# Performance work log

Hardware: AMD Instinct MI355X
Metric: run time of the kernel (lower is better)

The kernel has to match this reference:

```python
import jax, jax.numpy as jnp
import numpy as np

N, C, T = 8, 256, 512
H, KQ, OUT = 8, 256, 256
EPS = 1e-5


def sym_linear(x, w, stride):
    # w: (2, out_dim); circulant-grouped expansion to (2T, out_dim), then x @ cp
    out_dim = w.shape[1]
    idx = (jnp.arange(out_dim)[None, :] - jnp.arange(T)[:, None] * stride) % out_dim  # (T, out_dim)
    cp = w[:, idx].transpose(1, 0, 2).reshape(2 * T, out_dim)  # cat of rolled copies
    return x @ cp


def ln2d(x, g, b):
    # LayerNorm over last two dims (T, 2T) with affine params (T, 2T)
    mu = jnp.mean(x, axis=(-2, -1), keepdims=True)
    var = jnp.mean(jnp.square(x - mu), axis=(-2, -1), keepdims=True)
    return (x - mu) / jnp.sqrt(var + EPS) * g + b


def setup_inputs() -> dict:
    key = jax.random.key(0)
    ks = jax.random.split(key, 16)
    stdv = 1.0 / np.sqrt(2 * T)
    u = lambda k, shape, s: jax.random.uniform(k, shape, jnp.float32, -s, s)
    return {
        "x": jax.random.normal(ks[0], (N, C, T), jnp.float32),
        "Wq": u(ks[1], (KQ, C), 1.0 / np.sqrt(C)),
        "Wk": u(ks[2], (KQ, C), 1.0 / np.sqrt(C)),
        "Wv": u(ks[3], (OUT, C), 1.0 / np.sqrt(C)),
        "m1w0": u(ks[4], (2, 2 * T), stdv),
        "m2w0": u(ks[5], (2, 2 * T), stdv),
        "m1w1": u(ks[6], (2, 2 * T), stdv),
        "m2w1": u(ks[7], (2, T), stdv),
        "ln1g0": 1.0 + 0.1 * jax.random.normal(ks[8], (T, 2 * T), jnp.float32),
        "ln1b0": 0.1 * jax.random.normal(ks[9], (T, 2 * T), jnp.float32),
        "ln2g0": 1.0 + 0.1 * jax.random.normal(ks[10], (T, 2 * T), jnp.float32),
        "ln2b0": 0.1 * jax.random.normal(ks[11], (T, 2 * T), jnp.float32),
        "ln1g1": 1.0 + 0.1 * jax.random.normal(ks[12], (T, 2 * T), jnp.float32),
        "ln1b1": 0.1 * jax.random.normal(ks[13], (T, 2 * T), jnp.float32),
    }


def reference(x, Wq, Wk, Wv, m1w0, m2w0, m1w1, m2w1,
              ln1g0, ln1b0, ln2g0, ln2b0, ln1g1, ln1b1):
    dk = KQ // H
    q = jnp.einsum('oc,nct->not', Wq, x).reshape(N, H, dk, T).transpose(0, 1, 3, 2)  # (N,H,T,dk)
    k = jnp.einsum('oc,nct->not', Wk, x).reshape(N, H, dk, T)                        # (N,H,dk,T)
    v = jnp.einsum('oc,nct->not', Wv, x).reshape(N, H, OUT // H, T).transpose(0, 1, 3, 2)  # (N,H,T,dv)

    scores = jnp.einsum('nhtd,nhds->nhts', q, k) / np.sqrt(dk)  # (N,H,T,T)
    ar = jnp.arange(T, dtype=jnp.float32)
    pd = jnp.abs(ar[None, :] - ar[:, None]) / (T - 1)  # (T,T)
    p = jnp.stack([scores, jnp.broadcast_to(pd, scores.shape)], axis=-1)  # (N,H,T,T,2)
    p = p.reshape(N, H, T, 2 * T)

    def transpose_pairs(z):
        return z.reshape(N, H, T, T, 2).transpose(0, 1, 3, 2, 4)

    # mix block 0 (intermediate)
    p = ln2d(sym_linear(p, m1w0, 2), ln1g0, ln1b0)
    p = jax.nn.gelu(transpose_pairs(p), approximate=False).reshape(N, H, T, 2 * T)
    p = ln2d(sym_linear(p, m2w0, 2), ln2g0, ln2b0)
    p = jax.nn.gelu(transpose_pairs(p), approximate=False).reshape(N, H, T, 2 * T)

    # mix block 1 (final)
    p = ln2d(sym_linear(p, m1w1, 2), ln1g1, ln1b1)
    p = jax.nn.gelu(transpose_pairs(p), approximate=False).reshape(N, H, T, 2 * T)
    p = sym_linear(p, m2w1, 1)           # (N,H,T,T), out_roll_stride = T // T * 1
    p = p.transpose(0, 1, 3, 2)

    attn = jax.nn.softmax(p, axis=-1)
    out = jnp.einsum('nhts,nhsd->nhtd', attn, v)  # (N,H,T,dv)
    return out.transpose(0, 1, 3, 2).reshape(N, OUT, T)
```

## Files before the change

### kernel.cpp

```cpp
#include <hip/hip_runtime.h>
#include <hip/hip_bf16.h>
#include <math.h>

#define CDIM 256
#define TDIM 512
#define T2   1024
#define NB   64
#define MTOT 524288.0f

typedef __bf16 bf16x8 __attribute__((ext_vector_type(8)));
typedef float  f32x4  __attribute__((ext_vector_type(4)));
typedef ushort ushort8v __attribute__((ext_vector_type(8)));
typedef ushort ushort4v __attribute__((ext_vector_type(4)));

__device__ __forceinline__ ushort f2bf(float f) {
  union { float f; unsigned u; } v; v.f = f;
  unsigned r = v.u + 0x7fffu + ((v.u >> 16) & 1u);
  return (ushort)(r >> 16);
}
__device__ __forceinline__ float bf2f(ushort h) {
  union { unsigned u; float f; } v; v.u = ((unsigned)h) << 16;
  return v.f;
}
__device__ __forceinline__ float gelu_exact(float x) {
  return 0.5f * x * (1.0f + erff(x * 0.7071067811865475f));
}

#define TO_LDS(p)  ((__attribute__((address_space(3))) void*)(unsigned)(uintptr_t)(p))
#define TO_GLB(p)  ((const __attribute__((address_space(1))) void*)(uintptr_t)(p))
#define GLOAD_LDS16(g, l) __builtin_amdgcn_global_load_lds(TO_GLB(g), TO_LDS(l), 16, 0, 0)

#define BAR()    asm volatile("s_barrier" ::: "memory")
#define WAITL()  asm volatile("s_waitcnt lgkmcnt(0)" ::: "memory")
#define WAITV4() asm volatile("s_waitcnt vmcnt(4)" ::: "memory")
#define WAITV0() asm volatile("s_waitcnt vmcnt(0)" ::: "memory")

__global__ __launch_bounds__(256)
void proj_kernel(const float* __restrict__ x, const float* __restrict__ Wq,
                 const float* __restrict__ Wk, const float* __restrict__ Wv,
                 ushort* __restrict__ qb, ushort* __restrict__ kb,
                 float* __restrict__ vp) {
  int t = blockIdx.x * 256 + threadIdx.x;
  int o = blockIdx.y;
  int n = blockIdx.z;
  const float* xn = x + (long)n * CDIM * TDIM;
  float aq = 0.f, ak = 0.f, av = 0.f;
  for (int c = 0; c < CDIM; ++c) {
    float xv = xn[c * TDIM + t];
    aq = fmaf(Wq[o * CDIM + c], xv, aq);
    ak = fmaf(Wk[o * CDIM + c], xv, ak);
    av = fmaf(Wv[o * CDIM + c], xv, av);
  }
  int h = o >> 5, d = o & 31;
  long bidx = (((long)(n * 8 + h) * 512) + t) * 32 + d;
  qb[bidx] = f2bf(aq);
  kb[bidx] = f2bf(ak);
  vp[((long)n * 256 + o) * TDIM + t] = av;
}

__global__ __launch_bounds__(256)
void prep_kernel(const float* __restrict__ m1w0, const float* __restrict__ m2w0,
                 const float* __restrict__ m1w1, const float* __restrict__ m2w1,
                 ushort* __restrict__ cpte0, ushort* __restrict__ cpto0,
                 ushort* __restrict__ cpt1, ushort* __restrict__ cpt2,
                 ushort* __restrict__ cpt3, ushort* __restrict__ pdb) {
  long i = (long)blockIdx.x * 256 + threadIdx.x;
  if (i < 524288) {
    int o = (int)(i >> 9), s = (int)(i & 511);
    int idx = (o - 2 * s) & 1023;
    cpte0[i] = f2bf(m1w0[idx]);
    cpto0[i] = f2bf(m1w0[1024 + idx]);
  } else if (i < 1572864) {
    long j = i - 524288;
    int o = (int)(j >> 10), kk = (int)(j & 1023);
    cpt1[j] = f2bf(m2w0[(kk & 1) * 1024 + ((o - 2 * (kk >> 1)) & 1023)]);
  } else if (i < 2621440) {
    long j = i - 1572864;
    int o = (int)(j >> 10), kk = (int)(j & 1023);
    cpt2[j] = f2bf(m1w1[(kk & 1) * 1024 + ((o - 2 * (kk >> 1)) & 1023)]);
  } else if (i < 3145728) {
    long j = i - 2621440;
    int o = (int)(j >> 10), kk = (int)(j & 1023);
    cpt3[j] = f2bf(m2w1[(kk & 1) * 512 + ((o - (kk >> 1)) & 511)]);
  } else if (i < 3407872) {
    long j = i - 3145728;
    int t = (int)(j >> 9), s = (int)(j & 511);
    pdb[j] = f2bf(fabsf((float)(s - t)) * (1.0f / 511.0f));
  }
}

__global__ __launch_bounds__(256)
void prep2_kernel(const float* __restrict__ g0, const float* __restrict__ b0,
                  const float* __restrict__ g1, const float* __restrict__ b1,
                  const float* __restrict__ g2, const float* __restrict__ b2,
                  ushort* __restrict__ gbb0, ushort* __restrict__ gbb1,
                  ushort* __restrict__ gbb2) {
  long i = (long)blockIdx.x * 256 + threadIdx.x;
  int set = (int)(i >> 18);
  long j = i & 262143;
  const float* g = set == 0 ? g0 : (set == 1 ? g1 : g2);
  const float* b = set == 0 ? b0 : (set == 1 ? b1 : b2);
  ushort* gbb    = set == 0 ? gbb0 : (set == 1 ? gbb1 : gbb2);
  float2 gv = *(const float2*)(g + 2 * j);
  float2 bv = *(const float2*)(b + 2 * j);
  ushort4v o; o[0] = f2bf(gv.x); o[1] = f2bf(bv.x); o[2] = f2bf(gv.y); o[3] = f2bf(bv.y);
  *(ushort4v*)(gbb + 4 * j) = o;
}

__global__ __launch_bounds__(256)
void scores_kernel(const ushort* __restrict__ qb, const ushort* __restrict__ kb,
                   ushort* __restrict__ S) {
  int tb = blockIdx.x;
  int b  = blockIdx.y;
  int wv = threadIdx.x >> 6, lane = threadIdx.x & 63;
  int fr = lane & 15, fq = lane >> 4;
  int t0 = tb * 64 + wv * 16;
  bf16x8 af = *(const bf16x8*)(qb + ((long)b * 512 + t0 + fr) * 32 + fq * 8);
  const ushort* kbase = kb + (long)b * 512 * 32 + fr * 32 + fq * 8;
  ushort* Sb = S + ((long)b * 512 + t0 + fq * 4) * 512 + fr;
  f32x4 zz = {0.f, 0.f, 0.f, 0.f};
#pragma unroll 4
  for (int st = 0; st < 32; ++st) {
    bf16x8 bfv = *(const bf16x8*)(kbase + st * 512);
    f32x4 acc = __builtin_amdgcn_mfma_f32_16x16x32_bf16(af, bfv, zz, 0, 0, 0);
#pragma unroll
    for (int r = 0; r < 4; ++r)
      Sb[(long)r * 512 + st * 16] = f2bf(acc[r] * 0.17677669529663687f);
  }
}

#define LDS_BUF  65536
#define LDS_BOFF 32768

#define STAGE_A_(buf, h, kt) do { \
  const ushort* gA0_ = Ab + (long)((h)*128 +      sr0) * K + (kt)*64 + slog8; \
  const ushort* gA1_ = Ab + (long)((h)*128 + 64 + sr0) * K + (kt)*64 + slog8; \
  char* dA_ = ldsw + (size_t)(buf) * LDS_BUF + (h)*16384 + tid*16; \
  GLOAD_LDS16(gA0_, dA_); GLOAD_LDS16(gA1_, dA_ + 8192); } while(0)

#define STAGE_B_(buf, h, kt) do { \
  const ushort* gB0_ = Bb + (long)((h)*128 +      sr0) * K + (kt)*64 + slog8; \
  const ushort* gB1_ = Bb + (long)((h)*128 + 64 + sr0) * K + (kt)*64 + slog8; \
  char* dB_ = ldsw + (size_t)(buf) * LDS_BUF + LDS_BOFF + (h)*16384 + tid*16; \
  GLOAD_LDS16(gB0_, dB_); GLOAD_LDS16(gB1_, dB_ + 8192); } while(0)

#define LD_A_(buf, mh) do { \
  const char* aB_ = ldsc + (size_t)(buf) * LDS_BUF; \
  _Pragma("unroll") for (int mi = 0; mi < 4; ++mi) { \
    int ar_ = wm*128 + (mh)*64 + mi*16 + fr; \
    const char* rb_ = aB_ + ar_*128; int sw_ = (ar_&7)<<4; \
    af[mi][0] = *(const bf16x8*)(rb_ + ((fq*16) ^ sw_)); \
    af[mi][1] = *(const bf16x8*)(rb_ + ((64 + fq*16) ^ sw_)); \
  } } while(0)

#define LD_B_(dst, buf, nh) do { \
  const char* bB_ = ldsc + (size_t)(buf) * LDS_BUF + LDS_BOFF; \
  _Pragma("unroll") for (int ni = 0; ni < 2; ++ni) { \
    int br_ = wn*64 + (nh)*32 + ni*16 + fr; \
    const char* rb_ = bB_ + br_*128; int sw_ = (br_&7)<<4; \
    dst[ni][0] = *(const bf16x8*)(rb_ + ((fq*16) ^ sw_)); \
    dst[ni][1] = *(const bf16x8*)(rb_ + ((64 + fq*16) ^ sw_)); \
  } } while(0)

#define QUAD_(mh, nh, bfa) do { \
  __builtin_amdgcn_s_setprio(1); \
  _Pragma("unroll") for (int kk = 0; kk < 2; ++kk) \
  _Pragma("unroll") for (int mi = 0; mi < 4; ++mi) \
  _Pragma("unroll") for (int ni = 0; ni < 2; ++ni) \
    acc[(mh)*4+mi][(nh)*2+ni] = __builtin_amdgcn_mfma_f32_16x16x32_bf16( \
        af[mi][kk], bfa[ni][kk], acc[(mh)*4+mi][(nh)*2+ni], 0, 0, 0); \
  __builtin_amdgcn_s_setprio(0); } while(0)

template<int K, bool FINAL>
__global__ __launch_bounds__(512, 2)
void gemm256_kernel(const ushort* __restrict__ A, long aStride,
                    const ushort* __restrict__ BT, long bStride,
                    void* __restrict__ Out, int ncols, float* __restrict__ stats,
                    const float* __restrict__ Cadd) {
  __shared__ ushort lds[2][2][256 * 64];
  const int tid = threadIdx.x;
  const int bm = blockIdx.x, bn = blockIdx.y, b = blockIdx.z;
  constexpr int NKT2 = K >> 7;
  const ushort* Ab = A  + (long)b * aStride + (long)bm * 256 * K;
  const ushort* Bb = BT + (long)b * bStride + (long)bn * 256 * K;
  const int lane = tid & 63;
  const int fr = lane & 15, fq = lane >> 4;
  const int wid = tid >> 6, wm = wid >> 2, wn = wid & 3;
  const int sr0 = tid >> 3;
  const int slog8 = ((tid & 7) ^ (sr0 & 7)) * 8;
  const char* ldsc = (const char*)&lds[0][0][0];
  char*       ldsw = (char*)&lds[0][0][0];

  f32x4 acc[8][4] = {};
  bf16x8 af[4][2], bf0[2][2], bf1[2][2];

  STAGE_B_(0, 0, 0); STAGE_B_(0, 1, 0);
  STAGE_A_(0, 0, 0); STAGE_A_(0, 1, 0);
  STAGE_B_(1, 0, 1); STAGE_B_(1, 1, 1);
  WAITV4();
  BAR();

  for (int i = 0; i < NKT2; ++i) {
    const int t1 = 2 * i + 1, t2 = 2 * i + 2, t3 = 2 * i + 3;
    const bool st = (i < NKT2 - 1);
    LD_A_(0, 0); LD_B_(bf0, 0, 0); LD_B_(bf1, 0, 1);
    STAGE_A_(1, 0, t1); STAGE_A_(1, 1, t1);
    BAR(); WAITL();
    QUAD_(0, 0, bf0); QUAD_(0, 1, bf1);
    BAR();
    LD_A_(0, 1);
    if (st) { STAGE_B_(0, 0, t2); STAGE_B_(0, 1, t2); WAITV4(); } else { WAITV0(); }
    BAR(); WAITL();
    QUAD_(1, 1, bf1); QUAD_(1, 0, bf0);
    BAR();
    LD_A_(1, 0); LD_B_(bf0, 1, 0); LD_B_(bf1, 1, 1);
    if (st) { STAGE_A_(0, 0, t2); STAGE_A_(0, 1, t2); }
    BAR(); WAITL();
    QUAD_(0, 0, bf0); QUAD_(0, 1, bf1);
    BAR();
    LD_A_(1, 1);
    if (st) { STAGE_B_(1, 0, t3); STAGE_B_(1, 1, t3); WAITV4(); }
    BAR(); WAITL();
    QUAD_(1, 1, bf1); QUAD_(1, 0, bf0);
    BAR();
  }

  const int r0 = bm * 256 + wm * 128;
  const int c0 = bn * 256 + wn * 64;
  if (!FINAL) {
    ushort* Yb = (ushort*)Out + (long)b * 512 * ncols;
    float s1 = 0.f, s2 = 0.f;
#pragma unroll
    for (int mi = 0; mi < 8; ++mi)
#pragma unroll
      for (int ni = 0; ni < 4; ++ni)
#pragma unroll
        for (int r = 0; r < 4; ++r) {
          float v = acc[mi][ni][r];
          int row = r0 + mi * 16 + fq * 4 + r;
          int col = c0 + ni * 16 + fr;
          if (Cadd) v += Cadd[(long)row * ncols + col];
          s1 += v; s2 += v * v;
          Yb[(long)row * ncols + col] = f2bf(v);
        }
    __syncthreads();
    float* red = (float*)&lds[0][0][0];
    red[tid] = s1; red[tid + 512] = s2;
    __syncthreads();
    for (int off = 256; off > 0; off >>= 1) {
      if (tid < off) { red[tid] += red[tid + off]; red[512 + tid] += red[512 + tid + off]; }
      __syncthreads();
    }
    if (tid == 0) {
      atomicAdd(&stats[b * 2],     red[0]);
      atomicAdd(&stats[b * 2 + 1], red[512]);
    }
  } else {
    float* Lb = (float*)Out + (long)b * 512 * ncols;
#pragma unroll
    for (int mi = 0; mi < 8; ++mi)
#pragma unroll
      for (int ni = 0; ni < 4; ++ni)
#pragma unroll
        for (int r = 0; r < 4; ++r) {
          int row = r0 + mi * 16 + fq * 4 + r;
          int col = c0 + ni * 16 + fr;
          Lb[(long)row * ncols + col] = acc[mi][ni][r];
        }
  }
}

__global__ __launch_bounds__(256)
void apply_kernel(const ushort* __restrict__ Y, const float* __restrict__ stats,
                  const ushort* __restrict__ gbb, ushort* __restrict__ P) {
  __shared__ ushort2 tile[32][65];
  int ti = blockIdx.x;
  int si = blockIdx.y;
  int b  = blockIdx.z;
  float mu  = stats[b * 2] * (1.0f / MTOT);
  float var = stats[b * 2 + 1] * (1.0f / MTOT) - mu * mu;
  float rstd = rsqrtf(var + 1e-5f);
  const ushort* Yb = Y + (long)b * 512 * 1024;
  int tr  = threadIdx.x >> 4;
  int sp4 = (threadIdx.x & 15) * 4;
#pragma unroll
  for (int pass = 0; pass < 2; ++pass) {
    int t  = ti * 32 + pass * 16 + tr;
    int sp = si * 64 + sp4;
    ushort8v yv  = *(const ushort8v*)(Yb + (long)t * 1024 + 2 * sp);
    ushort8v gbA = *(const ushort8v*)(gbb + ((long)t * 512 + sp) * 4);
    ushort8v gbB = *(const ushort8v*)(gbb + ((long)t * 512 + sp + 2) * 4);
#pragma unroll
    for (int j = 0; j < 4; ++j) {
      int base = (j & 1) * 4;
      ushort gg0 = (j < 2) ? gbA[base + 0] : gbB[base + 0];
      ushort bb0 = (j < 2) ? gbA[base + 1] : gbB[base + 1];
      ushort gg1 = (j < 2) ? gbA[base + 2] : gbB[base + 2];
      ushort bb1 = (j < 2) ? gbA[base + 3] : gbB[base + 3];
      float y0 = (bf2f(yv[2 * j])     - mu) * rstd * bf2f(gg0) + bf2f(bb0);
      float y1 = (bf2f(yv[2 * j + 1]) - mu) * rstd * bf2f(gg1) + bf2f(bb1);
      ushort2 o; o.x = f2bf(gelu_exact(y0)); o.y = f2bf(gelu_exact(y1));
      tile[pass * 16 + tr][sp4 + j] = o;
    }
  }
  __syncthreads();
  ushort* Pb = P + (long)b * 512 * 1024;
  int srow = threadIdx.x >> 3;
  int t4   = (threadIdx.x & 7) * 4;
#pragma unroll
  for (int pass = 0; pass < 2; ++pass) {
    int scol = pass * 32 + srow;
    int s = si * 64 + scol;
    ushort2 v0 = tile[t4 + 0][scol];
    ushort2 v1 = tile[t4 + 1][scol];
    ushort2 v2 = tile[t4 + 2][scol];
    ushort2 v3 = tile[t4 + 3][scol];
    int tcol0 = ti * 32 + t4;
    ushort8v w2 = {v0.x, v0.y, v1.x, v1.y, v2.x, v2.y, v3.x, v3.y};
    *(ushort8v*)(Pb + (long)s * 1024 + 2 * tcol0) = w2;
  }
}

__global__ __launch_bounds__(256)
void smax_av_kernel(const float* __restrict__ L, const float* __restrict__ vp,
                    float* __restrict__ out) {
  __shared__ float Lt[32][513];
  int bh = blockIdx.x;
  int at = blockIdx.y;
  int n = bh >> 3, h = bh & 7;
  int wv = threadIdx.x >> 6, lane = threadIdx.x & 63;
  for (int rr = 0; rr < 8; ++rr) {
    int row = wv * 8 + rr;
    int a = at * 32 + row;
    const float* Lr = L + ((long)bh * 512 + a) * 512;
    float e[8];
#pragma unroll
    for (int j = 0; j < 8; ++j) e[j] = Lr[j * 64 + lane];
    float m = e[0];
#pragma unroll
    for (int j = 1; j < 8; ++j) m = fmaxf(m, e[j]);
    for (int off = 32; off > 0; off >>= 1) m = fmaxf(m, __shfl_xor(m, off, 64));
    float s = 0.f;
#pragma unroll
    for (int j = 0; j < 8; ++j) { e[j] = expf(e[j] - m); s += e[j]; }
    for (int off = 32; off > 0; off >>= 1) s += __shfl_xor(s, off, 64);
    float inv = 1.0f / s;
#pragma unroll
    for (int j = 0; j < 8; ++j) Lt[row][j * 64 + lane] = e[j] * inv;
  }
  __syncthreads();
  int r  = threadIdx.x & 31;
  int d0 = (threadIdx.x >> 5) * 4;
  const float* vb = vp + ((long)n * 256 + h * 32) * 512;
  float a0 = 0.f, a1 = 0.f, a2 = 0.f, a3 = 0.f;
  for (int bc = 0; bc < 512; bc += 4) {
    float4 v0 = *(const float4*)(vb + (d0 + 0) * 512 + bc);
    float4 v1 = *(const float4*)(vb + (d0 + 1) * 512 + bc);
    float4 v2 = *(const float4*)(vb + (d0 + 2) * 512 + bc);
    float4 v3 = *(const float4*)(vb + (d0 + 3) * 512 + bc);
    float p0 = Lt[r][bc], p1 = Lt[r][bc + 1], p2 = Lt[r][bc + 2], p3 = Lt[r][bc + 3];
    a0 = fmaf(p0, v0.x, fmaf(p1, v0.y, fmaf(p2, v0.z, fmaf(p3, v0.w, a0))));
    a1 = fmaf(p0, v1.x, fmaf(p1, v1.y, fmaf(p2, v1.z, fmaf(p3, v1.w, a1))));
    a2 = fmaf(p0, v2.x, fmaf(p1, v2.y, fmaf(p2, v2.z, fmaf(p3, v2.w, a2))));
    a3 = fmaf(p0, v3.x, fmaf(p1, v3.y, fmaf(p2, v3.z, fmaf(p3, v3.w, a3))));
  }
  int a = at * 32 + r;
  float* ob = out + ((long)n * 256 + h * 32) * 512;
  ob[(d0 + 0) * 512 + a] = a0;
  ob[(d0 + 1) * 512 + a] = a1;
  ob[(d0 + 2) * 512 + a] = a2;
  ob[(d0 + 3) * 512 + a] = a3;
}

extern "C" void kernel_launch(void* const* d_in, const int* in_sizes, int n_in,
                              void* d_out, int out_size, void* d_ws, size_t ws_size,
                              hipStream_t stream) {
  const float* x     = (const float*)d_in[0];
  const float* Wq    = (const float*)d_in[1];
  const float* Wk    = (const float*)d_in[2];
  const float* Wv    = (const float*)d_in[3];
  const float* m1w0  = (const float*)d_in[4];
  const float* m2w0  = (const float*)d_in[5];
  const float* m1w1  = (const float*)d_in[6];
  const float* m2w1  = (const float*)d_in[7];
  const float* ln1g0 = (const float*)d_in[8];
  const float* ln1b0 = (const float*)d_in[9];
  const float* ln2g0 = (const float*)d_in[10];
  const float* ln2b0 = (const float*)d_in[11];
  const float* ln1g1 = (const float*)d_in[12];
  const float* ln1b1 = (const float*)d_in[13];

  char* w = (char*)d_ws;
  float*  vp     = (float*) (w + 0);
  ushort* qb     = (ushort*)(w + (4ull  << 20));
  ushort* kb     = (ushort*)(w + (6ull  << 20));
  float*  stats  = (float*) (w + (8ull  << 20));
  ushort* cpte0  = (ushort*)(w + (9ull  << 20));
  ushort* cpto0  = (ushort*)(w + (10ull << 20));
  ushort* cpt1   = (ushort*)(w + (11ull << 20));
  ushort* cpt2   = (ushort*)(w + (13ull << 20));
  ushort* cpt3   = (ushort*)(w + (15ull << 20));
  ushort* pdb    = (ushort*)(w + (16ull << 20));
  float*  pdpart = (float*) (w + (17ull << 20));
  ushort* bufA   = (ushort*)(w + (20ull << 20));
  ushort* bufB   = (ushort*)(w + (84ull << 20));
  ushort* gbb0   = qb;
  ushort* gbb1   = kb;
  ushort* gbb2   = cpte0;
  ushort* S      = bufA;
  float*  L      = (float*)bufB;
  float*  outp   = (float*)d_out;

  hipMemsetAsync(stats, 0, 3 * NB * 2 * sizeof(float), stream);

  proj_kernel<<<dim3(2, 256, 8), 256, 0, stream>>>(x, Wq, Wk, Wv, qb, kb, vp);
  prep_kernel<<<13312, 256, 0, stream>>>(m1w0, m2w0, m1w1, m2w1,
                                         cpte0, cpto0, cpt1, cpt2, cpt3, pdb);
  scores_kernel<<<dim3(8, 64), 256, 0, stream>>>(qb, kb, S);
  gemm256_kernel<512, true><<<dim3(2, 4, 1), 512, 0, stream>>>(
      pdb, 0, cpto0, 0, pdpart, 1024, nullptr, nullptr);
  gemm256_kernel<512, false><<<dim3(2, 4, 64), 512, 0, stream>>>(
      S, 512L * 512, cpte0, 0, bufB, 1024, stats, pdpart);
  prep2_kernel<<<3072, 256, 0, stream>>>(ln1g0, ln1b0, ln2g0, ln2b0, ln1g1, ln1b1,
                                         gbb0, gbb1, gbb2);
  apply_kernel<<<dim3(16, 8, 64), 256, 0, stream>>>(bufB, stats, gbb0, bufA);
  gemm256_kernel<1024, false><<<dim3(2, 4, 64), 512, 0, stream>>>(
      bufA, 512L * 1024, cpt1, 0, bufB, 1024, stats + 128, nullptr);
  apply_kernel<<<dim3(16, 8, 64), 256, 0, stream>>>(bufB, stats + 128, gbb1, bufA);
  gemm256_kernel<1024, false><<<dim3(2, 4, 64), 512, 0, stream>>>(
      bufA, 512L * 1024, cpt2, 0, bufB, 1024, stats + 256, nullptr);
  apply_kernel<<<dim3(16, 8, 64), 256, 0, stream>>>(bufB, stats + 256, gbb2, bufA);
  gemm256_kernel<1024, true><<<dim3(2, 2, 64), 512, 0, stream>>>(
      cpt3, 0, bufA, 512L * 1024, L, 512, nullptr, nullptr);
  smax_av_kernel<<<dim3(64, 16), 256, 0, stream>>>(L, vp, outp);
}
```

Baseline: 513.6 us.

## Compute positional partial analytically, stage score stores via LDS, vectorize softmax loads

The positional-distance GEMM (pdb times the odd circulant weights) is replaced by a small kernel that builds pdpart with a prefix-sum recurrence over the circulant weights. This drops the pdb buffer and one GEMM launch, and the recurrence runs in fp32 instead of bf16 inputs. The scores kernel now writes each wave's MFMA outputs into swizzled LDS and then emits coalesced 16-byte rows, replacing scattered 2-byte global stores. The softmax kernel loads each row with float4 vectors, so each lane now holds contiguous columns. The pdpart kernel runs on only 4 blocks with a serial loop of 512 steps, which may sit on the critical path.

```diff
diff --git a/kernel.cpp b/kernel.cpp
--- a/kernel.cpp
+++ b/kernel.cpp
@@ -63,7 +63,7 @@
                  const float* __restrict__ m1w1, const float* __restrict__ m2w1,
                  ushort* __restrict__ cpte0, ushort* __restrict__ cpto0,
                  ushort* __restrict__ cpt1, ushort* __restrict__ cpt2,
-                 ushort* __restrict__ cpt3, ushort* __restrict__ pdb) {
+                 ushort* __restrict__ cpt3) {
   long i = (long)blockIdx.x * 256 + threadIdx.x;
   if (i < 524288) {
     int o = (int)(i >> 9), s = (int)(i & 511);
@@ -82,34 +82,35 @@
     long j = i - 2621440;
     int o = (int)(j >> 10), kk = (int)(j & 1023);
     cpt3[j] = f2bf(m2w1[(kk & 1) * 512 + ((o - (kk >> 1)) & 511)]);
-  } else if (i < 3407872) {
-    long j = i - 3145728;
-    int t = (int)(j >> 9), s = (int)(j & 511);
-    pdb[j] = f2bf(fabsf((float)(s - t)) * (1.0f / 511.0f));
-  }
-}
-
-__global__ __launch_bounds__(256)
-void prep2_kernel(const float* __restrict__ g0, const float* __restrict__ b0,
-                  const float* __restrict__ g1, const float* __restrict__ b1,
-                  const float* __restrict__ g2, const float* __restrict__ b2,
-                  ushort* __restrict__ gbb0, ushort* __restrict__ gbb1,
-                  ushort* __restrict__ gbb2) {
-  long i = (long)blockIdx.x * 256 + threadIdx.x;
-  int set = (int)(i >> 18);
-  long j = i & 262143;
-  const float* g = set == 0 ? g0 : (set == 1 ? g1 : g2);
-  const float* b = set == 0 ? b0 : (set == 1 ? b1 : b2);
-  ushort* gbb    = set == 0 ? gbb0 : (set == 1 ? gbb1 : gbb2);
-  float2 gv = *(const float2*)(g + 2 * j);
-  float2 bv = *(const float2*)(b + 2 * j);
-  ushort4v o; o[0] = f2bf(gv.x); o[1] = f2bf(bv.x); o[2] = f2bf(gv.y); o[3] = f2bf(bv.y);
-  *(ushort4v*)(gbb + 4 * j) = o;
+  }
+}
+
+__global__ __launch_bounds__(256)
+void pdpart_kernel(const float* __restrict__ m1w0, float* __restrict__ pdpart) {
+  __shared__ float W2[1024];
+  int o = blockIdx.x * 256 + threadIdx.x;
+  for (int i = threadIdx.x; i < 1024; i += 256) W2[i] = m1w0[1024 + i];
+  __syncthreads();
+  float P0 = 0.f, Tv = 0.f;
+  for (int s = 0; s < 512; ++s) {
+    float wv2 = W2[(o - 2 * s) & 1023];
+    P0 = fmaf((float)s, wv2, P0);
+    Tv += wv2;
+  }
+  float pd = P0 * (1.0f / 511.0f);
+  pdpart[o] = pd;
+  float P = 0.f;
+  for (int t = 0; t < 511; ++t) {
+    P += W2[(o - 2 * t) & 1023];
+    pd += (2.f * P - Tv) * (1.0f / 511.0f);
+    pdpart[(long)(t + 1) * 1024 + o] = pd;
+  }
 }
 
 __global__ __launch_bounds__(256)
 void scores_kernel(const ushort* __restrict__ qb, const ushort* __restrict__ kb,
                    ushort* __restrict__ S) {
+  __shared__ ushort sm[4 * 16 * 512];
   int tb = blockIdx.x;
   int b  = blockIdx.y;
   int wv = threadIdx.x >> 6, lane = threadIdx.x & 63;
@@ -117,15 +118,26 @@
   int t0 = tb * 64 + wv * 16;
   bf16x8 af = *(const bf16x8*)(qb + ((long)b * 512 + t0 + fr) * 32 + fq * 8);
   const ushort* kbase = kb + (long)b * 512 * 32 + fr * 32 + fq * 8;
-  ushort* Sb = S + ((long)b * 512 + t0 + fq * 4) * 512 + fr;
+  char* smw = (char*)sm + wv * 16384;
   f32x4 zz = {0.f, 0.f, 0.f, 0.f};
 #pragma unroll 4
   for (int st = 0; st < 32; ++st) {
     bf16x8 bfv = *(const bf16x8*)(kbase + st * 512);
     f32x4 acc = __builtin_amdgcn_mfma_f32_16x16x32_bf16(af, bfv, zz, 0, 0, 0);
 #pragma unroll
-    for (int r = 0; r < 4; ++r)
-      Sb[(long)r * 512 + st * 16] = f2bf(acc[r] * 0.17677669529663687f);
+    for (int r = 0; r < 4; ++r) {
+      int row = fq * 4 + r;
+      int byteoff = row * 1024 + (((st * 16 + fr) * 2) ^ ((row & 7) << 4));
+      *(ushort*)(smw + byteoff) = f2bf(acc[r] * 0.17677669529663687f);
+    }
+  }
+  __syncthreads();
+  ushort* Sb = S + ((long)b * 512 + t0) * 512;
+#pragma unroll
+  for (int j = 0; j < 16; ++j) {
+    int byteoff = j * 1024 + ((lane * 16) ^ ((j & 7) << 4));
+    ushort8v v = *(const ushort8v*)(smw + byteoff);
+    *(ushort8v*)(Sb + (long)j * 512 + lane * 8) = v;
   }
 }
 
@@ -322,6 +334,24 @@
 }
 
 __global__ __launch_bounds__(256)
+void prep2_kernel(const float* __restrict__ g0, const float* __restrict__ b0,
+                  const float* __restrict__ g1, const float* __restrict__ b1,
+                  const float* __restrict__ g2, const float* __restrict__ b2,
+                  ushort* __restrict__ gbb0, ushort* __restrict__ gbb1,
+                  ushort* __restrict__ gbb2) {
+  long i = (long)blockIdx.x * 256 + threadIdx.x;
+  int set = (int)(i >> 18);
+  long j = i & 262143;
+  const float* g = set == 0 ? g0 : (set == 1 ? g1 : g2);
+  const float* b = set == 0 ? b0 : (set == 1 ? b1 : b2);
+  ushort* gbb    = set == 0 ? gbb0 : (set == 1 ? gbb1 : gbb2);
+  float2 gv = *(const float2*)(g + 2 * j);
+  float2 bv = *(const float2*)(b + 2 * j);
+  ushort4v o; o[0] = f2bf(gv.x); o[1] = f2bf(bv.x); o[2] = f2bf(gv.y); o[3] = f2bf(bv.y);
+  *(ushort4v*)(gbb + 4 * j) = o;
+}
+
+__global__ __launch_bounds__(256)
 void smax_av_kernel(const float* __restrict__ L, const float* __restrict__ vp,
                     float* __restrict__ out) {
   __shared__ float Lt[32][513];
@@ -332,10 +362,10 @@
   for (int rr = 0; rr < 8; ++rr) {
     int row = wv * 8 + rr;
     int a = at * 32 + row;
-    const float* Lr = L + ((long)bh * 512 + a) * 512;
-    float e[8];
-#pragma unroll
-    for (int j = 0; j < 8; ++j) e[j] = Lr[j * 64 + lane];
+    const float* Lr = L + ((long)bh * 512 + a) * 512 + lane * 8;
+    float4 va = *(const float4*)(Lr);
+    float4 vb4 = *(const float4*)(Lr + 4);
+    float e[8] = {va.x, va.y, va.z, va.w, vb4.x, vb4.y, vb4.z, vb4.w};
     float m = e[0];
 #pragma unroll
     for (int j = 1; j < 8; ++j) m = fmaxf(m, e[j]);
@@ -346,7 +376,7 @@
     for (int off = 32; off > 0; off >>= 1) s += __shfl_xor(s, off, 64);
     float inv = 1.0f / s;
 #pragma unroll
-    for (int j = 0; j < 8; ++j) Lt[row][j * 64 + lane] = e[j] * inv;
+    for (int j = 0; j < 8; ++j) Lt[row][lane * 8 + j] = e[j] * inv;
   }
   __syncthreads();
   int r  = threadIdx.x & 31;
@@ -400,7 +430,6 @@
   ushort* cpt1   = (ushort*)(w + (11ull << 20));
   ushort* cpt2   = (ushort*)(w + (13ull << 20));
   ushort* cpt3   = (ushort*)(w + (15ull << 20));
-  ushort* pdb    = (ushort*)(w + (16ull << 20));
   float*  pdpart = (float*) (w + (17ull << 20));
   ushort* bufA   = (ushort*)(w + (20ull << 20));
   ushort* bufB   = (ushort*)(w + (84ull << 20));
@@ -414,11 +443,10 @@
   hipMemsetAsync(stats, 0, 3 * NB * 2 * sizeof(float), stream);
 
   proj_kernel<<<dim3(2, 256, 8), 256, 0, stream>>>(x, Wq, Wk, Wv, qb, kb, vp);
-  prep_kernel<<<13312, 256, 0, stream>>>(m1w0, m2w0, m1w1, m2w1,
-                                         cpte0, cpto0, cpt1, cpt2, cpt3, pdb);
+  prep_kernel<<<12288, 256, 0, stream>>>(m1w0, m2w0, m1w1, m2w1,
+                                         cpte0, cpto0, cpt1, cpt2, cpt3);
+  pdpart_kernel<<<4, 256, 0, stream>>>(m1w0, pdpart);
   scores_kernel<<<dim3(8, 64), 256, 0, stream>>>(qb, kb, S);
-  gemm256_kernel<512, true><<<dim3(2, 4, 1), 512, 0, stream>>>(
-      pdb, 0, cpto0, 0, pdpart, 1024, nullptr, nullptr);
   gemm256_kernel<512, false><<<dim3(2, 4, 64), 512, 0, stream>>>(
       S, 512L * 512, cpte0, 0, bufB, 1024, stats, pdpart);
   prep2_kernel<<<3072, 256, 0, stream>>>(ln1g0, ln1b0, ln2g0, ln2b0, ln1g1, ln1b1,
```

New measurement: 521.4 us, median of 2. About the same (+1.5%).
